# Optimization experiments

Hardware: AMD Instinct MI355X
Metric: run time of the kernel (lower is better)

Reference implementation:

```python
import jax, jax.numpy as jnp
import numpy as np

# dims: N patches, D_IN input feats, D model, DI=inner, DS=state, DC=conv, DTR=dt_rank
N, D_IN, D, DI, DS, DC, DTR, NC, NL = 4096, 1024, 512, 1024, 16, 4, 32, 4, 2


def setup_inputs() -> dict:
    key = jax.random.key(0)
    ks = jax.random.split(key, 16)
    g = lambda i, shape, s=0.02: jax.random.normal(ks[i], shape, dtype=jnp.float32) * s
    return {
        "data_s": jax.random.normal(ks[0], (N, 512), dtype=jnp.float32),
        "data_l": jax.random.normal(ks[1], (N, 512), dtype=jnp.float32),
        "coord_s": jax.random.uniform(ks[2], (N, 2), dtype=jnp.float32) * 1000.0,
        "label": jax.random.randint(ks[3], (1,), 0, NC),
        "fc1_w": g(4, (D, D_IN)), "fc1_b": jnp.zeros((D,), jnp.float32),
        "ln_w": jnp.ones((NL, D), jnp.float32), "ln_b": jnp.zeros((NL, D), jnp.float32),
        "in_proj_w": g(5, (NL, 2 * DI, D)),
        "conv_w": g(6, (NL, DI, DC), 0.1), "conv_b": jnp.zeros((NL, DI), jnp.float32),
        "x_proj_w": g(7, (NL, DTR + 2 * DS, DI)),
        "dt_proj_w": g(8, (NL, DI, DTR), 0.1), "dt_proj_b": g(9, (NL, DI), 0.5),
        "A_log": jnp.broadcast_to(jnp.log(jnp.arange(1, DS + 1, dtype=jnp.float32)), (NL, DI, DS)) + jnp.zeros((NL, DI, DS), jnp.float32),
        "D_param": jnp.ones((NL, DI), jnp.float32),
        "out_proj_w": g(10, (NL, D, DI)),
        "norm_w": jnp.ones((D,), jnp.float32), "norm_b": jnp.zeros((D,), jnp.float32),
        "attn_w1": g(11, (128, D)), "attn_b1": jnp.zeros((128,), jnp.float32),
        "attn_w2": g(12, (1, 128)), "attn_b2": jnp.zeros((1,), jnp.float32),
        "cls_w": g(13, (NC, D)), "cls_b": jnp.zeros((NC,), jnp.float32),
    }


def _layer_norm(x, w, b, eps=1e-5):
    m = x.mean(-1, keepdims=True)
    v = ((x - m) ** 2).mean(-1, keepdims=True)
    return (x - m) * jax.lax.rsqrt(v + eps) * w + b


def _mamba(h, inw, cw, cb, xpw, dtw, dtb, Alog, Dp, ow):
    # h: (B, L, D) -> (B, L, D); canonical Mamba block (mamba_ssm defaults)
    B, L, _ = h.shape
    xz = h @ inw.T                      # (B, L, 2*DI)
    x, z = jnp.split(xz, 2, axis=-1)
    # causal depthwise conv1d, kernel DC, left pad DC-1 (== torch pad+truncate)
    xp = jnp.pad(x, ((0, 0), (DC - 1, 0), (0, 0)))
    x = sum(xp[:, k:k + L, :] * cw[:, k] for k in range(DC)) + cb
    x = jax.nn.silu(x)
    xdbl = x @ xpw.T                    # (B, L, DTR + 2*DS)
    dt, Bm, Cm = jnp.split(xdbl, [DTR, DTR + DS], axis=-1)
    dt = jax.nn.softplus(dt @ dtw.T + dtb)   # (B, L, DI)
    A = -jnp.exp(Alog)                  # (DI, DS)
    dA = jnp.exp(dt[..., None] * A)                          # (B, L, DI, DS)
    dBx = dt[..., None] * Bm[:, :, None, :] * x[..., None]   # (B, L, DI, DS)

    def step(hst, inp):
        dA_t, dBx_t, C_t = inp
        hst = dA_t * hst + dBx_t        # (B, DI, DS)
        return hst, jnp.einsum('bds,bs->bd', hst, C_t)

    h0 = jnp.zeros((B, DI, DS), x.dtype)
    _, ys = jax.lax.scan(step, h0, (jnp.swapaxes(dA, 0, 1), jnp.swapaxes(dBx, 0, 1), jnp.swapaxes(Cm, 0, 1)))
    y = jnp.swapaxes(ys, 0, 1) + Dp * x
    return (y * jax.nn.silu(z)) @ ow.T


def _forward(data_s, data_l, coord_s, fc1_w, fc1_b, ln_w, ln_b, in_proj_w, conv_w, conv_b,
             x_proj_w, dt_proj_w, dt_proj_b, A_log, D_param, out_proj_w, norm_w, norm_b,
             attn_w1, attn_b1, attn_w2, attn_b2, cls_w, cls_b, label):
    h = jnp.concatenate([data_s, data_l], axis=1)            # (N, 1024)
    packed = jnp.concatenate([h, coord_s], axis=1)[None]     # (1, N, 1026)
    h = packed[:, :, :-2]                                    # strip coords
    h = jax.nn.relu(h @ fc1_w.T + fc1_b)                     # dropout: eval mode (identity)
    for i in range(NL):
        res = h
        hn = _layer_norm(h, ln_w[i], ln_b[i])
        h = _mamba(hn, in_proj_w[i], conv_w[i], conv_b[i], x_proj_w[i], dt_proj_w[i],
                   dt_proj_b[i], A_log[i], D_param[i], out_proj_w[i]) + res
    h = _layer_norm(h, norm_w, norm_b)
    A = jnp.tanh(h @ attn_w1.T + attn_b1) @ attn_w2.T + attn_b2   # (1, N, 1)
    A = jax.nn.softmax(jnp.swapaxes(A, 1, 2), axis=-1)            # (1, 1, N)
    hp = (A @ h)[0]                                               # (1, D)
    logits = hp @ cls_w.T + cls_b                                 # (1, NC)
    hz = jax.nn.sigmoid(logits)
    p = jnp.clip(hz, 1e-6, 1.0 - 1e-6)
    lce = jnp.log(p) - jnp.log1p(-p)                              # torch.logit
    Y_prob = jax.nn.softmax(lce, axis=1)
    loss = -jnp.take(jax.nn.log_softmax(lce, axis=1)[0], label[0])
    return lce, Y_prob, loss


def reference(data_s, data_l, coord_s, label, fc1_w, fc1_b, ln_w, ln_b, in_proj_w, conv_w,
              conv_b, x_proj_w, dt_proj_w, dt_proj_b, A_log, D_param, out_proj_w, norm_w,
              norm_b, attn_w1, attn_b1, attn_w2, attn_b2, cls_w, cls_b):
    return _forward(data_s, data_l, coord_s, fc1_w, fc1_b, ln_w, ln_b, in_proj_w, conv_w,
                    conv_b, x_proj_w, dt_proj_w, dt_proj_b, A_log, D_param, out_proj_w,
                    norm_w, norm_b, attn_w1, attn_b1, attn_w2, attn_b2, cls_w, cls_b, label)
```

## Files before the change

kernel.cpp:

```cpp
#include <hip/hip_runtime.h>
#include <math.h>

#define L_SEQ 4096
#define DMODEL 512
#define DIN    1024
#define DI     1024
#define DS     16
#define DC     4
#define DTR    32
#define NCHK   256
#define CL     16

typedef __bf16 bf16x8 __attribute__((ext_vector_type(8)));
typedef __bf16 bf16x4 __attribute__((ext_vector_type(4)));
typedef float floatx4 __attribute__((ext_vector_type(4)));

__device__ __forceinline__ void gl2lds16(const __bf16* g, __bf16* l) {
    __builtin_amdgcn_global_load_lds(
        (const __attribute__((address_space(1))) void*)g,
        (__attribute__((address_space(3))) void*)l, 16, 0, 0);
}

template <int BN, int ACT, bool BIAS, bool ADDDEST, bool OUTBF>
__global__ __launch_bounds__(256) void gemm_mfma(
    const __bf16* __restrict__ A, int lda,
    const __bf16* __restrict__ W, int ldw,
    const float* __restrict__ bias,
    float* __restrict__ C, __bf16* __restrict__ Cb, int ldc, int K)
{
    __shared__ __align__(16) __bf16 sA[128 * 32];
    __shared__ __align__(16) __bf16 sB[BN * 32];
    const int tid = threadIdx.x;
    const int wid = tid >> 6, lane = tid & 63;
    const int m0 = blockIdx.y * 128, n0 = blockIdx.x * BN;

    constexpr int MR = (BN == 128) ? 4 : 2;
    constexpr int NR = 4;
    const int wrow = (BN == 128) ? (wid >> 1) * 64 : wid * 32;
    const int wcol = (BN == 128) ? (wid & 1) * 64 : 0;

    const int srowA0 = wid * 32 + (lane >> 2);
    const int scol   = (lane & 3) * 8;
    const __bf16* aSrc0 = A + (size_t)(m0 + srowA0) * lda + scol;
    const __bf16* aSrc1 = aSrc0 + 16 * (size_t)lda;
    __bf16* aDst0 = &sA[wid * 1024];
    __bf16* aDst1 = &sA[wid * 1024 + 512];

    const __bf16* bSrc0;
    const __bf16* bSrc1 = nullptr;
    __bf16* bDst0;
    __bf16* bDst1 = nullptr;
    if (BN == 128) {
        bSrc0 = W + (size_t)(n0 + wid * 32 + (lane >> 2)) * ldw + scol;
        bSrc1 = bSrc0 + 16 * (size_t)ldw;
        bDst0 = &sB[wid * 1024];
        bDst1 = &sB[wid * 1024 + 512];
    } else {
        bSrc0 = W + (size_t)(n0 + wid * 16 + (lane >> 2)) * ldw + scol;
        bDst0 = &sB[wid * 512];
    }

    floatx4 acc[MR][NR] = {};
    const int fr = lane & 15;
    const int fk = (lane >> 4) * 8;

    for (int k0 = 0; k0 < K; k0 += 32) {
        __syncthreads();
        gl2lds16(aSrc0 + k0, aDst0);
        gl2lds16(aSrc1 + k0, aDst1);
        gl2lds16(bSrc0 + k0, bDst0);
        if (BN == 128) gl2lds16(bSrc1 + k0, bDst1);
        __syncthreads();
        bf16x8 af[MR], bfv[NR];
#pragma unroll
        for (int i = 0; i < MR; ++i)
            af[i] = *(const bf16x8*)&sA[(wrow + i * 16 + fr) * 32 + fk];
#pragma unroll
        for (int j = 0; j < NR; ++j)
            bfv[j] = *(const bf16x8*)&sB[(wcol + j * 16 + fr) * 32 + fk];
#pragma unroll
        for (int i = 0; i < MR; ++i)
#pragma unroll
            for (int j = 0; j < NR; ++j)
                acc[i][j] = __builtin_amdgcn_mfma_f32_16x16x32_bf16(
                    af[i], bfv[j], acc[i][j], 0, 0, 0);
    }

#pragma unroll
    for (int i = 0; i < MR; ++i)
#pragma unroll
        for (int j = 0; j < NR; ++j) {
            const int n = n0 + wcol + j * 16 + fr;
            float bv = 0.f;
            if (BIAS) bv = bias[n];
#pragma unroll
            for (int r = 0; r < 4; ++r) {
                const int m = m0 + wrow + i * 16 + (lane >> 4) * 4 + r;
                float v = acc[i][j][r] + bv;
                if (ACT == 1) v = fmaxf(v, 0.f);
                const size_t idx = (size_t)m * ldc + n;
                if (OUTBF) {
                    Cb[idx] = (__bf16)v;
                } else {
                    if (ADDDEST) v += C[idx];
                    C[idx] = v;
                }
            }
        }
}

template <int ACT, bool BIAS, bool OUTBF>
__global__ __launch_bounds__(256) void gemm_bt(
    const float* __restrict__ A, int lda,
    const float* __restrict__ W,
    const float* __restrict__ bias,
    float* __restrict__ C, __bf16* __restrict__ Cb, int ldc, int K)
{
    __shared__ float sA[16][68];
    __shared__ float sB[16][68];
    const int tid = threadIdx.x;
    const int tx = tid & 15, ty = tid >> 4;
    const int m0 = blockIdx.y * 64, n0 = blockIdx.x * 64;
    const int lr = tid >> 2;
    const int lk = (tid & 3) << 2;
    float acc[4][4] = {};
    const float* Ap = A + (size_t)(m0 + lr) * lda + lk;
    const float* Wp = W + (size_t)(n0 + lr) * K + lk;
    for (int k0 = 0; k0 < K; k0 += 16) {
        float4 a4 = *(const float4*)(Ap + k0);
        float4 b4 = *(const float4*)(Wp + k0);
        __syncthreads();
        sA[lk + 0][lr] = a4.x; sA[lk + 1][lr] = a4.y;
        sA[lk + 2][lr] = a4.z; sA[lk + 3][lr] = a4.w;
        sB[lk + 0][lr] = b4.x; sB[lk + 1][lr] = b4.y;
        sB[lk + 2][lr] = b4.z; sB[lk + 3][lr] = b4.w;
        __syncthreads();
#pragma unroll
        for (int kk = 0; kk < 16; ++kk) {
            float4 av = *(const float4*)&sA[kk][ty << 2];
            float4 bv = *(const float4*)&sB[kk][tx << 2];
            float am[4] = {av.x, av.y, av.z, av.w};
            float bm[4] = {bv.x, bv.y, bv.z, bv.w};
#pragma unroll
            for (int i = 0; i < 4; ++i)
#pragma unroll
                for (int j = 0; j < 4; ++j)
                    acc[i][j] = fmaf(am[i], bm[j], acc[i][j]);
        }
    }
#pragma unroll
    for (int i = 0; i < 4; ++i) {
        int m = m0 + (ty << 2) + i;
#pragma unroll
        for (int j = 0; j < 4; ++j) {
            int n = n0 + (tx << 2) + j;
            float v = acc[i][j];
            if (BIAS) v += bias[n];
            if (ACT == 1) v = fmaxf(v, 0.f);
            else if (ACT == 2) v = tanhf(v);
            else if (ACT == 3) v = (v > 20.f) ? v : log1pf(__expf(v));
            if (OUTBF) Cb[(size_t)m * ldc + n] = (__bf16)v;
            else       C[(size_t)m * ldc + n] = v;
        }
    }
}

__global__ void f2b4_k(const float* __restrict__ s0, __bf16* __restrict__ d0, int n0,
                       const float* __restrict__ s1, __bf16* __restrict__ d1, int n1,
                       const float* __restrict__ s2, __bf16* __restrict__ d2, int n2,
                       const float* __restrict__ s3, __bf16* __restrict__ d3, int n3)
{
    int i = blockIdx.x * 256 + threadIdx.x;
    const float* s; __bf16* d; int base;
    if (i < n0) { s = s0; d = d0; base = i; }
    else if (i < n0 + n1) { s = s1; d = d1; base = i - n0; }
    else if (i < n0 + n1 + n2) { s = s2; d = d2; base = i - n0 - n1; }
    else if (i < n0 + n1 + n2 + n3) { s = s3; d = d3; base = i - n0 - n1 - n2; }
    else return;
    float4 a = ((const float4*)s)[2 * base], b = ((const float4*)s)[2 * base + 1];
    bf16x8 v;
    v[0] = (__bf16)a.x; v[1] = (__bf16)a.y; v[2] = (__bf16)a.z; v[3] = (__bf16)a.w;
    v[4] = (__bf16)b.x; v[5] = (__bf16)b.y; v[6] = (__bf16)b.z; v[7] = (__bf16)b.w;
    *(bf16x8*)&d[8 * base] = v;
}

__global__ void concat_bf_k(const float* __restrict__ a,
                            const float* __restrict__ b,
                            __bf16* __restrict__ o)
{
    int idx = blockIdx.x * 256 + threadIdx.x;
    int m = idx >> 7, c8 = (idx & 127) << 3;
    const float* src = (c8 < 512) ? &a[(m << 9) + c8] : &b[(m << 9) + c8 - 512];
    float4 x = ((const float4*)src)[0], y = ((const float4*)src)[1];
    bf16x8 v;
    v[0] = (__bf16)x.x; v[1] = (__bf16)x.y; v[2] = (__bf16)x.z; v[3] = (__bf16)x.w;
    v[4] = (__bf16)y.x; v[5] = (__bf16)y.y; v[6] = (__bf16)y.z; v[7] = (__bf16)y.w;
    *(bf16x8*)&o[idx << 3] = v;
}

template <bool OB>
__global__ __launch_bounds__(128) void layernorm_k(
    const float* __restrict__ X, const float* __restrict__ w,
    const float* __restrict__ b, float* __restrict__ Yf, __bf16* __restrict__ Yb)
{
    const int r = blockIdx.x, tid = threadIdx.x;
    const size_t base = ((size_t)r << 9) + (tid << 2);
    const float4 v = *(const float4*)&X[base];
    float s = v.x + v.y + v.z + v.w;
#pragma unroll
    for (int o = 32; o; o >>= 1) s += __shfl_down(s, o, 64);
    __shared__ float red[2];
    if ((tid & 63) == 0) red[tid >> 6] = s;
    __syncthreads();
    const float mean = (red[0] + red[1]) * (1.f / 512.f);
    float dx = v.x - mean, dy = v.y - mean, dz = v.z - mean, dw = v.w - mean;
    float q = dx * dx + dy * dy + dz * dz + dw * dw;
#pragma unroll
    for (int o = 32; o; o >>= 1) q += __shfl_down(q, o, 64);
    __shared__ float red2[2];
    if ((tid & 63) == 0) red2[tid >> 6] = q;
    __syncthreads();
    const float rs = rsqrtf((red2[0] + red2[1]) * (1.f / 512.f) + 1e-5f);
    const float4 wv = *(const float4*)&w[tid << 2];
    const float4 bv = *(const float4*)&b[tid << 2];
    float o0 = dx * rs * wv.x + bv.x;
    float o1 = dy * rs * wv.y + bv.y;
    float o2 = dz * rs * wv.z + bv.z;
    float o3 = dw * rs * wv.w + bv.w;
    if (OB) {
        bf16x4 ov; ov[0] = (__bf16)o0; ov[1] = (__bf16)o1;
        ov[2] = (__bf16)o2; ov[3] = (__bf16)o3;
        *(bf16x4*)&Yb[base] = ov;
    } else {
        float4 ov; ov.x = o0; ov.y = o1; ov.z = o2; ov.w = o3;
        *(float4*)&Yf[base] = ov;
    }
}

__global__ void conv_silu_k(const __bf16* __restrict__ XZb,
                            const float* __restrict__ cw,
                            const float* __restrict__ cb,
                            __bf16* __restrict__ XCb)
{
    int i = blockIdx.x * 256 + threadIdx.x;
    int t = i >> 8, d4 = (i & 255) << 2;
    float wt[4][4];
#pragma unroll
    for (int d = 0; d < 4; ++d) {
        float4 w = *(const float4*)&cw[(d4 + d) << 2];
        wt[d][0] = w.x; wt[d][1] = w.y; wt[d][2] = w.z; wt[d][3] = w.w;
    }
    float4 c = *(const float4*)&cb[d4];
    float a0 = c.x, a1 = c.y, a2 = c.z, a3 = c.w;
#pragma unroll
    for (int k = 0; k < 4; ++k) {
        int ts = t + k - 3;
        if (ts >= 0) {
            bf16x4 x = *(const bf16x4*)&XZb[((size_t)ts << 11) + d4];
            a0 = fmaf((float)x[0], wt[0][k], a0);
            a1 = fmaf((float)x[1], wt[1][k], a1);
            a2 = fmaf((float)x[2], wt[2][k], a2);
            a3 = fmaf((float)x[3], wt[3][k], a3);
        }
    }
    a0 *= 1.f / (1.f + __expf(-a0));
    a1 *= 1.f / (1.f + __expf(-a1));
    a2 *= 1.f / (1.f + __expf(-a2));
    a3 *= 1.f / (1.f + __expf(-a3));
    bf16x4 ob; ob[0] = (__bf16)a0; ob[1] = (__bf16)a1;
    ob[2] = (__bf16)a2; ob[3] = (__bf16)a3;
    *(bf16x4*)&XCb[((size_t)t << 10) + d4] = ob;
}

__global__ __launch_bounds__(256) void scanA_k(
    const __bf16* __restrict__ dt, const __bf16* __restrict__ xc,
    const float* __restrict__ xdbl, const float* __restrict__ Alog,
    __bf16* __restrict__ sP, __bf16* __restrict__ sH)
{
    const int d = blockIdx.x * 256 + threadIdx.x;
    const int c = blockIdx.y;
    __shared__ float Bs[CL][DS];
    {
        int idx = threadIdx.x;
        int t = idx >> 4, s = idx & 15;
        Bs[t][s] = xdbl[(size_t)(c * CL + t) * 64 + 32 + s];
    }
    __syncthreads();
    float As[DS], h[DS];
#pragma unroll
    for (int s = 0; s < DS; ++s) {
        As[s] = -__expf(Alog[d * DS + s]);
        h[s] = 0.f;
    }
    float sumdt = 0.f;
    for (int t = 0; t < CL; ++t) {
        size_t tg = (size_t)(c * CL + t);
        float dtv = (float)dt[(tg << 10) + d];
        float xv  = (float)xc[(tg << 10) + d];
        float dx = dtv * xv;
        sumdt += dtv;
#pragma unroll
        for (int s = 0; s < DS; ++s) {
            float a = __expf(dtv * As[s]);
            h[s] = fmaf(a, h[s], dx * Bs[t][s]);
        }
    }
    size_t base = ((size_t)c * DI + d) * DS;
#pragma unroll
    for (int s = 0; s < DS; ++s) {
        sP[base + s] = (__bf16)__expf(As[s] * sumdt);
        sH[base + s] = (__bf16)h[s];
    }
}

__global__ __launch_bounds__(64) void scanB_k(
    const __bf16* __restrict__ sP, const __bf16* __restrict__ sH,
    __bf16* __restrict__ Hin)
{
    int p = blockIdx.x * 64 + threadIdx.x;
    float run = 0.f;
#pragma unroll 4
    for (int c = 0; c < NCHK; ++c) {
        size_t idx = (size_t)c * DI * DS + p;
        Hin[idx] = (__bf16)run;
        run = fmaf((float)sP[idx], run, (float)sH[idx]);
    }
}

__global__ __launch_bounds__(256) void scanC_k(
    const __bf16* __restrict__ dt, const __bf16* __restrict__ xc,
    const float* __restrict__ xdbl, const float* __restrict__ Alog,
    const float* __restrict__ Dp, const __bf16* __restrict__ XZb,
    const __bf16* __restrict__ Hin, __bf16* __restrict__ yz)
{
    const int d = blockIdx.x * 256 + threadIdx.x;
    const int c = blockIdx.y;
    __shared__ float Bs[CL][DS], Cs[CL][DS];
    {
        int idx = threadIdx.x;
        int t = idx >> 4, s = idx & 15;
        Bs[t][s] = xdbl[(size_t)(c * CL + t) * 64 + 32 + s];
        Cs[t][s] = xdbl[(size_t)(c * CL + t) * 64 + 48 + s];
    }
    __syncthreads();
    float As[DS], h[DS];
    size_t hbase = ((size_t)c * DI + d) * DS;
#pragma unroll
    for (int s = 0; s < DS; ++s) {
        As[s] = -__expf(Alog[d * DS + s]);
        h[s] = (float)Hin[hbase + s];
    }
    const float Dd = Dp[d];
    for (int t = 0; t < CL; ++t) {
        size_t tg = (size_t)(c * CL + t);
        float dtv = (float)dt[(tg << 10) + d];
        float xv  = (float)xc[(tg << 10) + d];
        float dx = dtv * xv;
        float y = 0.f;
#pragma unroll
        for (int s = 0; s < DS; ++s) {
            float a = __expf(dtv * As[s]);
            h[s] = fmaf(a, h[s], dx * Bs[t][s]);
            y = fmaf(h[s], Cs[t][s], y);
        }
        y = fmaf(Dd, xv, y);
        float zv = (float)XZb[(tg << 11) + 1024 + d];
        float sg = 1.f / (1.f + __expf(-zv));
        yz[(tg << 10) + d] = (__bf16)(y * (zv * sg));
    }
}

__global__ void score_k(const float* __restrict__ At,
                        const float* __restrict__ w2,
                        const float* __restrict__ b2,
                        float* __restrict__ sc)
{
    int t = blockIdx.x * 256 + threadIdx.x;
    const float4* a = (const float4*)(At + ((size_t)t << 7));
    const float4* w = (const float4*)w2;
    float acc = 0.f;
#pragma unroll
    for (int j = 0; j < 32; ++j) {
        float4 av = a[j], wv = w[j];
        acc += av.x * wv.x + av.y * wv.y + av.z * wv.z + av.w * wv.w;
    }
    sc[t] = acc + b2[0];
}

__global__ __launch_bounds__(256) void softmax_k(const float* __restrict__ s,
                                                 float* __restrict__ p)
{
    const int tid = threadIdx.x;
    float vals[16];
#pragma unroll
    for (int i = 0; i < 4; ++i) {
        float4 v = *(const float4*)&s[(tid << 4) + (i << 2)];
        vals[i * 4 + 0] = v.x; vals[i * 4 + 1] = v.y;
        vals[i * 4 + 2] = v.z; vals[i * 4 + 3] = v.w;
    }
    float mx = -1e30f;
#pragma unroll
    for (int i = 0; i < 16; ++i) mx = fmaxf(mx, vals[i]);
#pragma unroll
    for (int o = 32; o; o >>= 1) mx = fmaxf(mx, __shfl_xor(mx, o, 64));
    __shared__ float red[4];
    if ((tid & 63) == 0) red[tid >> 6] = mx;
    __syncthreads();
    mx = fmaxf(fmaxf(red[0], red[1]), fmaxf(red[2], red[3]));
    float sum = 0.f, e[16];
#pragma unroll
    for (int i = 0; i < 16; ++i) { e[i] = __expf(vals[i] - mx); sum += e[i]; }
#pragma unroll
    for (int o = 32; o; o >>= 1) sum += __shfl_xor(sum, o, 64);
    __syncthreads();
    if ((tid & 63) == 0) red[tid >> 6] = sum;
    __syncthreads();
    sum = red[0] + red[1] + red[2] + red[3];
    float inv = 1.f / sum;
#pragma unroll
    for (int i = 0; i < 4; ++i) {
        float4 ov;
        ov.x = e[i * 4 + 0] * inv; ov.y = e[i * 4 + 1] * inv;
        ov.z = e[i * 4 + 2] * inv; ov.w = e[i * 4 + 3] * inv;
        *(float4*)&p[(tid << 4) + (i << 2)] = ov;
    }
}

__global__ void pool_partial_k(const float* __restrict__ prob,
                               const float* __restrict__ hln,
                               float* __restrict__ part)
{
    int j = blockIdx.x * 256 + threadIdx.x;
    int c = blockIdx.y;
    float acc = 0.f;
    for (int t = c * 128; t < (c + 1) * 128; ++t)
        acc = fmaf(prob[t], hln[((size_t)t << 9) + j], acc);
    part[c * 512 + j] = acc;
}

__global__ void pool_reduce_k(const float* __restrict__ part,
                              float* __restrict__ hp)
{
    int j = blockIdx.x * 256 + threadIdx.x;
    float acc = 0.f;
    for (int c = 0; c < 32; ++c) acc += part[c * 512 + j];
    hp[j] = acc;
}

__global__ __launch_bounds__(256) void final_head_k(
    const float* __restrict__ hp, const float* __restrict__ cls_w,
    const float* __restrict__ cls_b, const int* __restrict__ label,
    float* __restrict__ out)
{
    const int w = threadIdx.x >> 6, lane = threadIdx.x & 63;
    float acc = 0.f;
    for (int k = lane; k < 512; k += 64) acc += hp[k] * cls_w[w * 512 + k];
#pragma unroll
    for (int o = 32; o; o >>= 1) acc += __shfl_down(acc, o, 64);
    __shared__ float lg[4];
    if (lane == 0) lg[w] = acc + cls_b[w];
    __syncthreads();
    if (threadIdx.x == 0) {
        float lce[4];
        for (int c = 0; c < 4; ++c) {
            float z = lg[c];
            float hz = 1.f / (1.f + expf(-z));
            float pc = fminf(fmaxf(hz, 1e-6f), 1.f - 1e-6f);
            lce[c] = logf(pc) - log1pf(-pc);
        }
        float mx = fmaxf(fmaxf(lce[0], lce[1]), fmaxf(lce[2], lce[3]));
        float se = 0.f;
        for (int c = 0; c < 4; ++c) se += expf(lce[c] - mx);
        for (int c = 0; c < 4; ++c) out[c] = lce[c];
        for (int c = 0; c < 4; ++c) out[4 + c] = expf(lce[c] - mx) / se;
        int lb = label[0];
        out[8] = -(lce[lb] - mx - logf(se));
    }
}

extern "C" void kernel_launch(void* const* d_in, const int* in_sizes, int n_in,
                              void* d_out, int out_size, void* d_ws, size_t ws_size,
                              hipStream_t stream)
{
    const float* data_s   = (const float*)d_in[0];
    const float* data_l   = (const float*)d_in[1];
    const int*   label    = (const int*)d_in[3];
    const float* fc1_w    = (const float*)d_in[4];
    const float* fc1_b    = (const float*)d_in[5];
    const float* ln_w     = (const float*)d_in[6];
    const float* ln_b     = (const float*)d_in[7];
    const float* in_proj_w= (const float*)d_in[8];
    const float* conv_w   = (const float*)d_in[9];
    const float* conv_b   = (const float*)d_in[10];
    const float* x_proj_w = (const float*)d_in[11];
    const float* dt_proj_w= (const float*)d_in[12];
    const float* dt_proj_b= (const float*)d_in[13];
    const float* A_log    = (const float*)d_in[14];
    const float* D_param  = (const float*)d_in[15];
    const float* out_proj_w=(const float*)d_in[16];
    const float* norm_w   = (const float*)d_in[17];
    const float* norm_b   = (const float*)d_in[18];
    const float* attn_w1  = (const float*)d_in[19];
    const float* attn_b1  = (const float*)d_in[20];
    const float* attn_w2  = (const float*)d_in[21];
    const float* attn_b2  = (const float*)d_in[22];
    const float* cls_w    = (const float*)d_in[23];
    const float* cls_b    = (const float*)d_in[24];
    float* out = (float*)d_out;

    float* ws = (float*)d_ws;
    size_t off = 0;
    float* h    = ws + off; off += (size_t)L_SEQ * DMODEL;
    float* hn   = ws + off; off += (size_t)L_SEQ * DMODEL;
    float* xdbl = ws + off; off += (size_t)L_SEQ * 64;
    float* At   = ws + off; off += (size_t)L_SEQ * 128;
    float* sc   = ws + off; off += L_SEQ;
    float* pb   = ws + off; off += L_SEQ;
    float* part = ws + off; off += 32 * 512;
    float* hp   = ws + off; off += 512;

    __bf16* bws = (__bf16*)(ws + off);
    size_t boff = 0;
    __bf16* Acatb = bws + boff; boff += (size_t)L_SEQ * DIN;
    __bf16* hnb   = bws + boff; boff += (size_t)L_SEQ * DMODEL;
    __bf16* XZb   = bws + boff; boff += (size_t)L_SEQ * 2 * DI;
    __bf16* XCb   = bws + boff; boff += (size_t)L_SEQ * DI;
    __bf16* dtbB  = bws + boff; boff += (size_t)L_SEQ * DI;
    __bf16* yzb   = bws + boff; boff += (size_t)L_SEQ * DI;
    __bf16* sPb   = bws + boff; boff += (size_t)NCHK * DI * DS;
    __bf16* sHb   = bws + boff; boff += (size_t)NCHK * DI * DS;
    __bf16* HinB  = bws + boff; boff += (size_t)NCHK * DI * DS;
    __bf16* wfc1b = bws + boff; boff += (size_t)DMODEL * DIN;
    __bf16* winb  = bws + boff; boff += (size_t)2 * 2 * DI * DMODEL;
    __bf16* wxpb  = bws + boff; boff += (size_t)2 * 64 * DI;
    __bf16* woutb = bws + boff; boff += (size_t)2 * DMODEL * DI;
    if (ws_size < off * sizeof(float) + boff * sizeof(__bf16)) return;

    const int n0 = DMODEL * DIN / 8;
    const int n1 = 2 * 2 * DI * DMODEL / 8;
    const int n2 = 2 * 64 * DI / 8;
    const int n3 = 2 * DMODEL * DI / 8;
    f2b4_k<<<(n0 + n1 + n2 + n3 + 255) / 256, 256, 0, stream>>>(
        fc1_w, wfc1b, n0, in_proj_w, winb, n1, x_proj_w, wxpb, n2, out_proj_w, woutb, n3);

    concat_bf_k<<<L_SEQ * DIN / 8 / 256, 256, 0, stream>>>(data_s, data_l, Acatb);
    gemm_mfma<64, 1, true, false, false><<<dim3(DMODEL / 64, L_SEQ / 128), 256, 0, stream>>>(
        Acatb, DIN, wfc1b, DIN, fc1_b, h, nullptr, DMODEL, DIN);

    for (int i = 0; i < 2; ++i) {
        const __bf16* inw = winb + (size_t)i * 2 * DI * DMODEL;
        const float* cwi = conv_w + (size_t)i * DI * DC;
        const float* cbi = conv_b + (size_t)i * DI;
        const __bf16* xpw = wxpb + (size_t)i * 64 * DI;
        const float* dtw = dt_proj_w + (size_t)i * DI * DTR;
        const float* dtbv= dt_proj_b + (size_t)i * DI;
        const float* Alg = A_log + (size_t)i * DI * DS;
        const float* Dpi = D_param + (size_t)i * DI;
        const __bf16* owi = woutb + (size_t)i * DMODEL * DI;

        layernorm_k<true><<<L_SEQ, 128, 0, stream>>>(h, ln_w + i * DMODEL, ln_b + i * DMODEL, nullptr, hnb);
        gemm_mfma<128, 0, false, false, true><<<dim3(2 * DI / 128, L_SEQ / 128), 256, 0, stream>>>(
            hnb, DMODEL, inw, DMODEL, nullptr, nullptr, XZb, 2 * DI, DMODEL);
        conv_silu_k<<<L_SEQ * DI / 4 / 256, 256, 0, stream>>>(XZb, cwi, cbi, XCb);
        gemm_mfma<64, 0, false, false, false><<<dim3(1, L_SEQ / 128), 256, 0, stream>>>(
            XCb, DI, xpw, DI, nullptr, xdbl, nullptr, 64, DI);
        gemm_bt<3, true, true><<<dim3(DI / 64, L_SEQ / 64), 256, 0, stream>>>(
            xdbl, 64, dtw, dtbv, nullptr, dtbB, DI, DTR);
        scanA_k<<<dim3(DI / 256, NCHK), 256, 0, stream>>>(dtbB, XCb, xdbl, Alg, sPb, sHb);
        scanB_k<<<DI * DS / 64, 64, 0, stream>>>(sPb, sHb, HinB);
        scanC_k<<<dim3(DI / 256, NCHK), 256, 0, stream>>>(dtbB, XCb, xdbl, Alg, Dpi, XZb, HinB, yzb);
        gemm_mfma<64, 0, false, true, false><<<dim3(DMODEL / 64, L_SEQ / 128), 256, 0, stream>>>(
            yzb, DI, owi, DI, nullptr, h, nullptr, DMODEL, DI);
    }

    layernorm_k<false><<<L_SEQ, 128, 0, stream>>>(h, norm_w, norm_b, hn, nullptr);
    gemm_bt<2, true, false><<<dim3(128 / 64, L_SEQ / 64), 256, 0, stream>>>(
        hn, DMODEL, attn_w1, attn_b1, At, nullptr, 128, DMODEL);
    score_k<<<L_SEQ / 256, 256, 0, stream>>>(At, attn_w2, attn_b2, sc);
    softmax_k<<<1, 256, 0, stream>>>(sc, pb);
    pool_partial_k<<<dim3(2, 32), 256, 0, stream>>>(pb, hn, part);
    pool_reduce_k<<<2, 256, 0, stream>>>(part, hp);
    final_head_k<<<1, 256, 0, stream>>>(hp, cls_w, cls_b, label, out);
}
```

Before: 442.2 us.

## Fuse dt projection into scan kernels and split-K the x_proj GEMM

Removes the separate dt_proj GEMM and its bf16 dt buffer: each scan kernel now recomputes softplus(xdbl[:, :32] @ dtw^T + b) per element from a transposed dt weight held in registers. The x_proj GEMM is split along K into four slabs to raise block count, and the scan kernels sum the partial slabs when loading. The MFMA GEMM also moves to a 64-wide K step per LDS stage, and conv_silu processes four timesteps per thread to reuse its loaded window. In exchange the dt math is computed twice (scanA and scanC), and the partial sums add extra reads.

Result: slower. 512.8 us (+16.0%).

```diff
diff --git a/kernel.cpp b/kernel.cpp
--- a/kernel.cpp
+++ b/kernel.cpp
@@ -10,6 +10,7 @@
 #define DTR    32
 #define NCHK   256
 #define CL     16
+#define SLAB   (L_SEQ * 64)
 
 typedef __bf16 bf16x8 __attribute__((ext_vector_type(8)));
 typedef __bf16 bf16x4 __attribute__((ext_vector_type(4)));
@@ -21,69 +22,82 @@
         (__attribute__((address_space(3))) void*)l, 16, 0, 0);
 }
 
-template <int BN, int ACT, bool BIAS, bool ADDDEST, bool OUTBF>
+template <int BN, int ACT, bool BIAS, bool ADDDEST, bool OUTBF, int KS>
 __global__ __launch_bounds__(256) void gemm_mfma(
     const __bf16* __restrict__ A, int lda,
     const __bf16* __restrict__ W, int ldw,
     const float* __restrict__ bias,
     float* __restrict__ C, __bf16* __restrict__ Cb, int ldc, int K)
 {
-    __shared__ __align__(16) __bf16 sA[128 * 32];
-    __shared__ __align__(16) __bf16 sB[BN * 32];
+    __shared__ __align__(16) __bf16 sA[128 * 64];
+    __shared__ __align__(16) __bf16 sB[BN * 64];
     const int tid = threadIdx.x;
     const int wid = tid >> 6, lane = tid & 63;
-    const int m0 = blockIdx.y * 128, n0 = blockIdx.x * BN;
+    const int m0 = blockIdx.y * 128;
+    int n0;
+    if (KS > 1) {
+        const int ksl = blockIdx.x;
+        A += (size_t)ksl * K;
+        W += (size_t)ksl * K;
+        C += (size_t)ksl * (size_t)gridDim.y * 128 * ldc;
+        n0 = 0;
+    } else {
+        n0 = blockIdx.x * BN;
+    }
 
     constexpr int MR = (BN == 128) ? 4 : 2;
     constexpr int NR = 4;
+    constexpr int BCH = (BN == 128) ? 4 : 2;
     const int wrow = (BN == 128) ? (wid >> 1) * 64 : wid * 32;
     const int wcol = (BN == 128) ? (wid & 1) * 64 : 0;
 
-    const int srowA0 = wid * 32 + (lane >> 2);
-    const int scol   = (lane & 3) * 8;
-    const __bf16* aSrc0 = A + (size_t)(m0 + srowA0) * lda + scol;
-    const __bf16* aSrc1 = aSrc0 + 16 * (size_t)lda;
-    __bf16* aDst0 = &sA[wid * 1024];
-    __bf16* aDst1 = &sA[wid * 1024 + 512];
-
-    const __bf16* bSrc0;
-    const __bf16* bSrc1 = nullptr;
-    __bf16* bDst0;
-    __bf16* bDst1 = nullptr;
-    if (BN == 128) {
-        bSrc0 = W + (size_t)(n0 + wid * 32 + (lane >> 2)) * ldw + scol;
-        bSrc1 = bSrc0 + 16 * (size_t)ldw;
-        bDst0 = &sB[wid * 1024];
-        bDst1 = &sB[wid * 1024 + 512];
-    } else {
-        bSrc0 = W + (size_t)(n0 + wid * 16 + (lane >> 2)) * ldw + scol;
-        bDst0 = &sB[wid * 512];
+    const int crow = lane >> 3;
+    const int ccol = (lane & 7) * 8;
+
+    const __bf16* aSrc[4];
+    __bf16* aDst[4];
+#pragma unroll
+    for (int q = 0; q < 4; ++q) {
+        const int r = wid * 32 + q * 8;
+        aSrc[q] = A + (size_t)(m0 + r + crow) * lda + ccol;
+        aDst[q] = &sA[r * 64];
+    }
+    const __bf16* bSrc[BCH];
+    __bf16* bDst[BCH];
+#pragma unroll
+    for (int q = 0; q < BCH; ++q) {
+        const int r = wid * (BN / 4) + q * 8;
+        bSrc[q] = W + (size_t)(n0 + r + crow) * ldw + ccol;
+        bDst[q] = &sB[r * 64];
     }
 
     floatx4 acc[MR][NR] = {};
     const int fr = lane & 15;
     const int fk = (lane >> 4) * 8;
 
-    for (int k0 = 0; k0 < K; k0 += 32) {
+    for (int k0 = 0; k0 < K; k0 += 64) {
         __syncthreads();
-        gl2lds16(aSrc0 + k0, aDst0);
-        gl2lds16(aSrc1 + k0, aDst1);
-        gl2lds16(bSrc0 + k0, bDst0);
-        if (BN == 128) gl2lds16(bSrc1 + k0, bDst1);
+#pragma unroll
+        for (int q = 0; q < 4; ++q) gl2lds16(aSrc[q] + k0, aDst[q]);
+#pragma unroll
+        for (int q = 0; q < BCH; ++q) gl2lds16(bSrc[q] + k0, bDst[q]);
         __syncthreads();
-        bf16x8 af[MR], bfv[NR];
-#pragma unroll
-        for (int i = 0; i < MR; ++i)
-            af[i] = *(const bf16x8*)&sA[(wrow + i * 16 + fr) * 32 + fk];
-#pragma unroll
-        for (int j = 0; j < NR; ++j)
-            bfv[j] = *(const bf16x8*)&sB[(wcol + j * 16 + fr) * 32 + fk];
-#pragma unroll
-        for (int i = 0; i < MR; ++i)
+#pragma unroll
+        for (int kk = 0; kk < 64; kk += 32) {
+            bf16x8 af[MR], bfv[NR];
+#pragma unroll
+            for (int i = 0; i < MR; ++i)
+                af[i] = *(const bf16x8*)&sA[(wrow + i * 16 + fr) * 64 + kk + fk];
 #pragma unroll
             for (int j = 0; j < NR; ++j)
-                acc[i][j] = __builtin_amdgcn_mfma_f32_16x16x32_bf16(
-                    af[i], bfv[j], acc[i][j], 0, 0, 0);
+                bfv[j] = *(const bf16x8*)&sB[(wcol + j * 16 + fr) * 64 + kk + fk];
+#pragma unroll
+            for (int i = 0; i < MR; ++i)
+#pragma unroll
+                for (int j = 0; j < NR; ++j)
+                    acc[i][j] = __builtin_amdgcn_mfma_f32_16x16x32_bf16(
+                        af[i], bfv[j], acc[i][j], 0, 0, 0);
+        }
     }
 
 #pragma unroll
@@ -158,7 +172,6 @@
             if (BIAS) v += bias[n];
             if (ACT == 1) v = fmaxf(v, 0.f);
             else if (ACT == 2) v = tanhf(v);
-            else if (ACT == 3) v = (v > 20.f) ? v : log1pf(__expf(v));
             if (OUTBF) Cb[(size_t)m * ldc + n] = (__bf16)v;
             else       C[(size_t)m * ldc + n] = v;
         }
@@ -182,6 +195,13 @@
     v[0] = (__bf16)a.x; v[1] = (__bf16)a.y; v[2] = (__bf16)a.z; v[3] = (__bf16)a.w;
     v[4] = (__bf16)b.x; v[5] = (__bf16)b.y; v[6] = (__bf16)b.z; v[7] = (__bf16)b.w;
     *(bf16x8*)&d[8 * base] = v;
+}
+
+__global__ void dtw_t_k(const float* __restrict__ src, float* __restrict__ dst)
+{
+    int i = blockIdx.x * 256 + threadIdx.x;
+    int l = i >> 15, rem = i & 32767, r = rem >> 5, k = rem & 31;
+    dst[l * 32768 + k * 1024 + r] = src[i];
 }
 
 __global__ void concat_bf_k(const float* __restrict__ a,
@@ -243,74 +263,126 @@
                             __bf16* __restrict__ XCb)
 {
     int i = blockIdx.x * 256 + threadIdx.x;
-    int t = i >> 8, d4 = (i & 255) << 2;
+    int t0 = (i >> 8) << 2, d4 = (i & 255) << 2;
     float wt[4][4];
 #pragma unroll
     for (int d = 0; d < 4; ++d) {
         float4 w = *(const float4*)&cw[(d4 + d) << 2];
         wt[d][0] = w.x; wt[d][1] = w.y; wt[d][2] = w.z; wt[d][3] = w.w;
     }
-    float4 c = *(const float4*)&cb[d4];
-    float a0 = c.x, a1 = c.y, a2 = c.z, a3 = c.w;
-#pragma unroll
-    for (int k = 0; k < 4; ++k) {
-        int ts = t + k - 3;
+    float4 cbv = *(const float4*)&cb[d4];
+    float win[7][4];
+#pragma unroll
+    for (int r = 0; r < 7; ++r) {
+        int ts = t0 - 3 + r;
         if (ts >= 0) {
             bf16x4 x = *(const bf16x4*)&XZb[((size_t)ts << 11) + d4];
-            a0 = fmaf((float)x[0], wt[0][k], a0);
-            a1 = fmaf((float)x[1], wt[1][k], a1);
-            a2 = fmaf((float)x[2], wt[2][k], a2);
-            a3 = fmaf((float)x[3], wt[3][k], a3);
-        }
-    }
-    a0 *= 1.f / (1.f + __expf(-a0));
-    a1 *= 1.f / (1.f + __expf(-a1));
-    a2 *= 1.f / (1.f + __expf(-a2));
-    a3 *= 1.f / (1.f + __expf(-a3));
-    bf16x4 ob; ob[0] = (__bf16)a0; ob[1] = (__bf16)a1;
-    ob[2] = (__bf16)a2; ob[3] = (__bf16)a3;
-    *(bf16x4*)&XCb[((size_t)t << 10) + d4] = ob;
+            win[r][0] = (float)x[0]; win[r][1] = (float)x[1];
+            win[r][2] = (float)x[2]; win[r][3] = (float)x[3];
+        } else {
+            win[r][0] = win[r][1] = win[r][2] = win[r][3] = 0.f;
+        }
+    }
+#pragma unroll
+    for (int u = 0; u < 4; ++u) {
+        float a0 = cbv.x, a1 = cbv.y, a2 = cbv.z, a3 = cbv.w;
+#pragma unroll
+        for (int k = 0; k < 4; ++k) {
+            a0 = fmaf(win[u + k][0], wt[0][k], a0);
+            a1 = fmaf(win[u + k][1], wt[1][k], a1);
+            a2 = fmaf(win[u + k][2], wt[2][k], a2);
+            a3 = fmaf(win[u + k][3], wt[3][k], a3);
+        }
+        a0 *= 1.f / (1.f + __expf(-a0));
+        a1 *= 1.f / (1.f + __expf(-a1));
+        a2 *= 1.f / (1.f + __expf(-a2));
+        a3 *= 1.f / (1.f + __expf(-a3));
+        bf16x4 ob; ob[0] = (__bf16)a0; ob[1] = (__bf16)a1;
+        ob[2] = (__bf16)a2; ob[3] = (__bf16)a3;
+        *(bf16x4*)&XCb[((size_t)(t0 + u) << 10) + d4] = ob;
+    }
 }
 
 __global__ __launch_bounds__(256) void scanA_k(
-    const __bf16* __restrict__ dt, const __bf16* __restrict__ xc,
-    const float* __restrict__ xdbl, const float* __restrict__ Alog,
+    const __bf16* __restrict__ xc, const float* __restrict__ xdblP,
+    const float* __restrict__ dtwT, const float* __restrict__ dtb,
+    const float* __restrict__ Alog,
     __bf16* __restrict__ sP, __bf16* __restrict__ sH)
 {
     const int d = blockIdx.x * 256 + threadIdx.x;
     const int c = blockIdx.y;
+    const int tid = threadIdx.x;
+    __shared__ float xlow[CL][DTR];
     __shared__ float Bs[CL][DS];
+#pragma unroll
+    for (int u = 0; u < 2; ++u) {
+        int idx = tid + u * 256;
+        int t = idx >> 5, k = idx & 31;
+        size_t g = (size_t)(c * CL + t) * 64 + k;
+        float v = xdblP[g] + xdblP[SLAB + g] + xdblP[2 * SLAB + g] + xdblP[3 * SLAB + g];
+        xlow[t][k] = v;
+    }
     {
-        int idx = threadIdx.x;
-        int t = idx >> 4, s = idx & 15;
-        Bs[t][s] = xdbl[(size_t)(c * CL + t) * 64 + 32 + s];
-    }
-    __syncthreads();
+        int t = tid >> 4, s = tid & 15;
+        size_t g = (size_t)(c * CL + t) * 64 + 32 + s;
+        Bs[t][s] = xdblP[g] + xdblP[SLAB + g] + xdblP[2 * SLAB + g] + xdblP[3 * SLAB + g];
+    }
+    __syncthreads();
+    float dtw_d[32];
+#pragma unroll
+    for (int k = 0; k < 32; ++k) dtw_d[k] = dtwT[k * 1024 + d];
+    const float dtb_d = dtb[d];
     float As[DS], h[DS];
-#pragma unroll
-    for (int s = 0; s < DS; ++s) {
-        As[s] = -__expf(Alog[d * DS + s]);
-        h[s] = 0.f;
-    }
+    {
+        const float4* Ap4 = (const float4*)&Alog[(size_t)d * DS];
+#pragma unroll
+        for (int q = 0; q < 4; ++q) {
+            float4 a = Ap4[q];
+            As[q * 4 + 0] = -__expf(a.x); As[q * 4 + 1] = -__expf(a.y);
+            As[q * 4 + 2] = -__expf(a.z); As[q * 4 + 3] = -__expf(a.w);
+        }
+    }
+#pragma unroll
+    for (int s = 0; s < DS; ++s) h[s] = 0.f;
     float sumdt = 0.f;
     for (int t = 0; t < CL; ++t) {
-        size_t tg = (size_t)(c * CL + t);
-        float dtv = (float)dt[(tg << 10) + d];
-        float xv  = (float)xc[(tg << 10) + d];
+        float acc = dtb_d;
+#pragma unroll
+        for (int k4 = 0; k4 < 8; ++k4) {
+            float4 xq = *(const float4*)&xlow[t][k4 * 4];
+            acc = fmaf(xq.x, dtw_d[k4 * 4 + 0], acc);
+            acc = fmaf(xq.y, dtw_d[k4 * 4 + 1], acc);
+            acc = fmaf(xq.z, dtw_d[k4 * 4 + 2], acc);
+            acc = fmaf(xq.w, dtw_d[k4 * 4 + 3], acc);
+        }
+        float dtv = (acc > 20.f) ? acc : log1pf(__expf(acc));
+        float xv = (float)xc[((size_t)(c * CL + t) << 10) + d];
         float dx = dtv * xv;
         sumdt += dtv;
+        float barr[16];
+#pragma unroll
+        for (int q = 0; q < 4; ++q) {
+            float4 b = *(const float4*)&Bs[t][q * 4];
+            barr[q * 4 + 0] = b.x; barr[q * 4 + 1] = b.y;
+            barr[q * 4 + 2] = b.z; barr[q * 4 + 3] = b.w;
+        }
 #pragma unroll
         for (int s = 0; s < DS; ++s) {
             float a = __expf(dtv * As[s]);
-            h[s] = fmaf(a, h[s], dx * Bs[t][s]);
+            h[s] = fmaf(a, h[s], dx * barr[s]);
         }
     }
     size_t base = ((size_t)c * DI + d) * DS;
-#pragma unroll
-    for (int s = 0; s < DS; ++s) {
-        sP[base + s] = (__bf16)__expf(As[s] * sumdt);
-        sH[base + s] = (__bf16)h[s];
-    }
+    bf16x8 p0, p1, h0, h1;
+#pragma unroll
+    for (int s = 0; s < 8; ++s) {
+        p0[s] = (__bf16)__expf(As[s] * sumdt);
+        p1[s] = (__bf16)__expf(As[s + 8] * sumdt);
+        h0[s] = (__bf16)h[s];
+        h1[s] = (__bf16)h[s + 8];
+    }
+    *(bf16x8*)&sP[base] = p0; *(bf16x8*)&sP[base + 8] = p1;
+    *(bf16x8*)&sH[base] = h0; *(bf16x8*)&sH[base + 8] = h1;
 }
 
 __global__ __launch_bounds__(64) void scanB_k(
@@ -328,40 +400,84 @@
 }
 
 __global__ __launch_bounds__(256) void scanC_k(
-    const __bf16* __restrict__ dt, const __bf16* __restrict__ xc,
-    const float* __restrict__ xdbl, const float* __restrict__ Alog,
-    const float* __restrict__ Dp, const __bf16* __restrict__ XZb,
-    const __bf16* __restrict__ Hin, __bf16* __restrict__ yz)
+    const __bf16* __restrict__ xc, const float* __restrict__ xdblP,
+    const float* __restrict__ dtwT, const float* __restrict__ dtb,
+    const float* __restrict__ Alog, const float* __restrict__ Dp,
+    const __bf16* __restrict__ XZb, const __bf16* __restrict__ Hin,
+    __bf16* __restrict__ yz)
 {
     const int d = blockIdx.x * 256 + threadIdx.x;
     const int c = blockIdx.y;
+    const int tid = threadIdx.x;
+    __shared__ float xlow[CL][DTR];
     __shared__ float Bs[CL][DS], Cs[CL][DS];
+#pragma unroll
+    for (int u = 0; u < 2; ++u) {
+        int idx = tid + u * 256;
+        int t = idx >> 5, k = idx & 31;
+        size_t g = (size_t)(c * CL + t) * 64 + k;
+        xlow[t][k] = xdblP[g] + xdblP[SLAB + g] + xdblP[2 * SLAB + g] + xdblP[3 * SLAB + g];
+    }
     {
-        int idx = threadIdx.x;
-        int t = idx >> 4, s = idx & 15;
-        Bs[t][s] = xdbl[(size_t)(c * CL + t) * 64 + 32 + s];
-        Cs[t][s] = xdbl[(size_t)(c * CL + t) * 64 + 48 + s];
-    }
-    __syncthreads();
+        int t = tid >> 4, s = tid & 15;
+        size_t g = (size_t)(c * CL + t) * 64 + 32 + s;
+        Bs[t][s] = xdblP[g] + xdblP[SLAB + g] + xdblP[2 * SLAB + g] + xdblP[3 * SLAB + g];
+        g += 16;
+        Cs[t][s] = xdblP[g] + xdblP[SLAB + g] + xdblP[2 * SLAB + g] + xdblP[3 * SLAB + g];
+    }
+    __syncthreads();
+    float dtw_d[32];
+#pragma unroll
+    for (int k = 0; k < 32; ++k) dtw_d[k] = dtwT[k * 1024 + d];
+    const float dtb_d = dtb[d];
     float As[DS], h[DS];
-    size_t hbase = ((size_t)c * DI + d) * DS;
-#pragma unroll
-    for (int s = 0; s < DS; ++s) {
-        As[s] = -__expf(Alog[d * DS + s]);
-        h[s] = (float)Hin[hbase + s];
+    {
+        const float4* Ap4 = (const float4*)&Alog[(size_t)d * DS];
+#pragma unroll
+        for (int q = 0; q < 4; ++q) {
+            float4 a = Ap4[q];
+            As[q * 4 + 0] = -__expf(a.x); As[q * 4 + 1] = -__expf(a.y);
+            As[q * 4 + 2] = -__expf(a.z); As[q * 4 + 3] = -__expf(a.w);
+        }
+    }
+    {
+        size_t hbase = ((size_t)c * DI + d) * DS;
+        bf16x8 h0 = *(const bf16x8*)&Hin[hbase];
+        bf16x8 h1 = *(const bf16x8*)&Hin[hbase + 8];
+#pragma unroll
+        for (int s = 0; s < 8; ++s) { h[s] = (float)h0[s]; h[s + 8] = (float)h1[s]; }
     }
     const float Dd = Dp[d];
     for (int t = 0; t < CL; ++t) {
+        float acc = dtb_d;
+#pragma unroll
+        for (int k4 = 0; k4 < 8; ++k4) {
+            float4 xq = *(const float4*)&xlow[t][k4 * 4];
+            acc = fmaf(xq.x, dtw_d[k4 * 4 + 0], acc);
+            acc = fmaf(xq.y, dtw_d[k4 * 4 + 1], acc);
+            acc = fmaf(xq.z, dtw_d[k4 * 4 + 2], acc);
+            acc = fmaf(xq.w, dtw_d[k4 * 4 + 3], acc);
+        }
+        float dtv = (acc > 20.f) ? acc : log1pf(__expf(acc));
         size_t tg = (size_t)(c * CL + t);
-        float dtv = (float)dt[(tg << 10) + d];
-        float xv  = (float)xc[(tg << 10) + d];
+        float xv = (float)xc[(tg << 10) + d];
         float dx = dtv * xv;
+        float barr[16], carr[16];
+#pragma unroll
+        for (int q = 0; q < 4; ++q) {
+            float4 b = *(const float4*)&Bs[t][q * 4];
+            float4 cc = *(const float4*)&Cs[t][q * 4];
+            barr[q * 4 + 0] = b.x; barr[q * 4 + 1] = b.y;
+            barr[q * 4 + 2] = b.z; barr[q * 4 + 3] = b.w;
+            carr[q * 4 + 0] = cc.x; carr[q * 4 + 1] = cc.y;
+            carr[q * 4 + 2] = cc.z; carr[q * 4 + 3] = cc.w;
+        }
         float y = 0.f;
 #pragma unroll
         for (int s = 0; s < DS; ++s) {
             float a = __expf(dtv * As[s]);
-            h[s] = fmaf(a, h[s], dx * Bs[t][s]);
-            y = fmaf(h[s], Cs[t][s], y);
+            h[s] = fmaf(a, h[s], dx * barr[s]);
+            y = fmaf(h[s], carr[s], y);
         }
         y = fmaf(Dd, xv, y);
         float zv = (float)XZb[(tg << 11) + 1024 + d];
@@ -510,14 +626,15 @@
 
     float* ws = (float*)d_ws;
     size_t off = 0;
-    float* h    = ws + off; off += (size_t)L_SEQ * DMODEL;
-    float* hn   = ws + off; off += (size_t)L_SEQ * DMODEL;
-    float* xdbl = ws + off; off += (size_t)L_SEQ * 64;
-    float* At   = ws + off; off += (size_t)L_SEQ * 128;
-    float* sc   = ws + off; off += L_SEQ;
-    float* pb   = ws + off; off += L_SEQ;
-    float* part = ws + off; off += 32 * 512;
-    float* hp   = ws + off; off += 512;
+    float* h     = ws + off; off += (size_t)L_SEQ * DMODEL;
+    float* hn    = ws + off; off += (size_t)L_SEQ * DMODEL;
+    float* xdblP = ws + off; off += (size_t)4 * SLAB;
+    float* dtwT  = ws + off; off += (size_t)2 * DTR * DI;
+    float* At    = ws + off; off += (size_t)L_SEQ * 128;
+    float* sc    = ws + off; off += L_SEQ;
+    float* pb    = ws + off; off += L_SEQ;
+    float* part  = ws + off; off += 32 * 512;
+    float* hp    = ws + off; off += 512;
 
     __bf16* bws = (__bf16*)(ws + off);
     size_t boff = 0;
@@ -525,7 +642,6 @@
     __bf16* hnb   = bws + boff; boff += (size_t)L_SEQ * DMODEL;
     __bf16* XZb   = bws + boff; boff += (size_t)L_SEQ * 2 * DI;
     __bf16* XCb   = bws + boff; boff += (size_t)L_SEQ * DI;
-    __bf16* dtbB  = bws + boff; boff += (size_t)L_SEQ * DI;
     __bf16* yzb   = bws + boff; boff += (size_t)L_SEQ * DI;
     __bf16* sPb   = bws + boff; boff += (size_t)NCHK * DI * DS;
     __bf16* sHb   = bws + boff; boff += (size_t)NCHK * DI * DS;
@@ -542,9 +658,10 @@
     const int n3 = 2 * DMODEL * DI / 8;
     f2b4_k<<<(n0 + n1 + n2 + n3 + 255) / 256, 256, 0, stream>>>(
         fc1_w, wfc1b, n0, in_proj_w, winb, n1, x_proj_w, wxpb, n2, out_proj_w, woutb, n3);
+    dtw_t_k<<<2 * DI * DTR / 256, 256, 0, stream>>>(dt_proj_w, dtwT);
 
     concat_bf_k<<<L_SEQ * DIN / 8 / 256, 256, 0, stream>>>(data_s, data_l, Acatb);
-    gemm_mfma<64, 1, true, false, false><<<dim3(DMODEL / 64, L_SEQ / 128), 256, 0, stream>>>(
+    gemm_mfma<64, 1, true, false, false, 1><<<dim3(DMODEL / 64, L_SEQ / 128), 256, 0, stream>>>(
         Acatb, DIN, wfc1b, DIN, fc1_b, h, nullptr, DMODEL, DIN);
 
     for (int i = 0; i < 2; ++i) {
@@ -552,24 +669,22 @@
         const float* cwi = conv_w + (size_t)i * DI * DC;
         const float* cbi = conv_b + (size_t)i * DI;
         const __bf16* xpw = wxpb + (size_t)i * 64 * DI;
-        const float* dtw = dt_proj_w + (size_t)i * DI * DTR;
+        const float* dtwTi = dtwT + (size_t)i * DTR * DI;
         const float* dtbv= dt_proj_b + (size_t)i * DI;
         const float* Alg = A_log + (size_t)i * DI * DS;
         const float* Dpi = D_param + (size_t)i * DI;
         const __bf16* owi = woutb + (size_t)i * DMODEL * DI;
 
         layernorm_k<true><<<L_SEQ, 128, 0, stream>>>(h, ln_w + i * DMODEL, ln_b + i * DMODEL, nullptr, hnb);
-        gemm_mfma<128, 0, false, false, true><<<dim3(2 * DI / 128, L_SEQ / 128), 256, 0, stream>>>(
+        gemm_mfma<128, 0, false, false, true, 1><<<dim3(2 * DI / 128, L_SEQ / 128), 256, 0, stream>>>(
             hnb, DMODEL, inw, DMODEL, nullptr, nullptr, XZb, 2 * DI, DMODEL);
-        conv_silu_k<<<L_SEQ * DI / 4 / 256, 256, 0, stream>>>(XZb, cwi, cbi, XCb);
-        gemm_mfma<64, 0, false, false, false><<<dim3(1, L_SEQ / 128), 256, 0, stream>>>(
-            XCb, DI, xpw, DI, nullptr, xdbl, nullptr, 64, DI);
-        gemm_bt<3, true, true><<<dim3(DI / 64, L_SEQ / 64), 256, 0, stream>>>(
-            xdbl, 64, dtw, dtbv, nullptr, dtbB, DI, DTR);
-        scanA_k<<<dim3(DI / 256, NCHK), 256, 0, stream>>>(dtbB, XCb, xdbl, Alg, sPb, sHb);
+        conv_silu_k<<<L_SEQ * DI / 16 / 256, 256, 0, stream>>>(XZb, cwi, cbi, XCb);
+        gemm_mfma<64, 0, false, false, false, 4><<<dim3(4, L_SEQ / 128), 256, 0, stream>>>(
+            XCb, DI, xpw, DI, nullptr, xdblP, nullptr, 64, DI / 4);
+        scanA_k<<<dim3(DI / 256, NCHK), 256, 0, stream>>>(XCb, xdblP, dtwTi, dtbv, Alg, sPb, sHb);
         scanB_k<<<DI * DS / 64, 64, 0, stream>>>(sPb, sHb, HinB);
-        scanC_k<<<dim3(DI / 256, NCHK), 256, 0, stream>>>(dtbB, XCb, xdbl, Alg, Dpi, XZb, HinB, yzb);
-        gemm_mfma<64, 0, false, true, false><<<dim3(DMODEL / 64, L_SEQ / 128), 256, 0, stream>>>(
+        scanC_k<<<dim3(DI / 256, NCHK), 256, 0, stream>>>(XCb, xdblP, dtwTi, dtbv, Alg, Dpi, XZb, HinB, yzb);
+        gemm_mfma<64, 0, false, true, false, 1><<<dim3(DMODEL / 64, L_SEQ / 128), 256, 0, stream>>>(
             yzb, DI, owi, DI, nullptr, h, nullptr, DMODEL, DI);
     }
 
```
